# Kernel optimization log

Hardware: AMD Instinct MI355X
Metric: run time of the kernel (lower is better)

## Reference

```python
import jax, jax.numpy as jnp
import numpy as np

B, S, D, F_DIM, E, TOP_K = 4, 2048, 1024, 1024, 8, 2


def setup_inputs() -> dict:
    key = jax.random.key(0)
    ks = jax.random.split(key, 6)
    return {
        "x": jax.random.normal(ks[0], (B, S, D), jnp.float32),
        "router_w": jax.random.normal(ks[1], (E, D), jnp.float32) * 0.02,
        "router_b": jax.random.normal(ks[2], (E,), jnp.float32) * 0.02,
        "expert_w": jax.random.normal(ks[3], (E, F_DIM, D), jnp.float32) * 0.02,
        "expert_b": jax.random.normal(ks[4], (E, F_DIM), jnp.float32) * 0.02,
        "expert_pref": jax.random.normal(ks[5], (E, D), jnp.float32),
        "top_k": TOP_K,
    }


def reference(x, router_w, router_b, expert_w, expert_b, expert_pref, top_k):
    num_experts = expert_w.shape[0]
    # Router: softmax over experts, then top-k with renormalization
    logits = jnp.einsum("bsd,ed->bse", x, router_w) + router_b
    routing_weights = jax.nn.softmax(logits, axis=-1)            # [B,S,E]
    top_w, top_idx = jax.lax.top_k(routing_weights, top_k)       # [B,S,K]
    top_w = top_w / jnp.sum(top_w, axis=-1, keepdims=True)
    # Dense per-expert combine weight: sum of renormalized top-k weights routed to each expert
    onehot = jax.nn.one_hot(top_idx, num_experts, dtype=x.dtype)  # [B,S,K,E]
    comb = jnp.einsum("bske,bsk->bse", onehot, top_w)             # [B,S,E]
    # Per-expert linear for every token, weighted combine (dense grouped-GEMM form)
    expert_out = jnp.einsum("bsd,efd->bsef", x, expert_w) + expert_b  # [B,S,E,F]
    final_output = jnp.einsum("bsef,bse->bsf", expert_out, comb)      # [B,S,F]
    # Expert utilization: fraction of tokens whose top-k contains expert i
    mask = jnp.sum(onehot, axis=2) > 0                            # [B,S,E]
    expert_utilization = jnp.mean(mask.astype(x.dtype), axis=(0, 1))
    # Load balance loss: MSE of mean routing weight vs ideal uniform usage
    usage = jnp.mean(routing_weights, axis=(0, 1))
    load_balance_loss = jnp.mean((usage - 1.0 / num_experts) ** 2)
    # Diversity: mean pairwise L2 distance over concatenated expert params (fixed small E)
    flat = jnp.concatenate(
        [expert_w.reshape(num_experts, -1), expert_b, expert_pref], axis=1
    )  # [E, P]
    dists = [jnp.linalg.norm(flat[i] - flat[j])
             for i in range(num_experts) for j in range(i + 1, num_experts)]
    diversity_score = jnp.mean(jnp.stack(dists))
    return final_output, routing_weights, expert_utilization, load_balance_loss, diversity_score
```

## Files before the change

kernel.cpp:

```cpp
#include <hip/hip_runtime.h>
#include <stdint.h>

typedef unsigned short u16;
typedef __attribute__((ext_vector_type(4))) float f32x4;
typedef __attribute__((ext_vector_type(8))) short bf16x8;

#define NTOK 8192
#define DDIM 1024
#define FDIM 1024
#define NEXP 8
#define PCAP 8192
#define RBLK 512

__device__ __align__(256) u16 g_xb[NTOK * DDIM];
__device__ __align__(256) u16 g_wbf[NEXP * FDIM * DDIM];
__device__ __align__(256) u16 g_buf0[NTOK * FDIM];
__device__ __align__(256) u16 g_buf1[NTOK * FDIM];
__device__ __align__(256) int g_ptok[NEXP * PCAP];
__device__ __align__(256) float g_pw[NEXP * PCAP];
__device__ __align__(256) unsigned g_e01[NTOK];
__device__ __align__(256) float g_w0[NTOK];
__device__ __align__(256) float g_w1[NTOK];
__device__ __align__(256) float g_usage_part[NEXP * RBLK];
__device__ __align__(256) float g_gram_part[36 * RBLK];
__device__ __align__(256) unsigned g_tile[160];
__device__ int g_cnt[16];

__device__ __forceinline__ u16 f2bf(float f) {
  unsigned u = __builtin_bit_cast(unsigned, f);
  unsigned r = u + 0x7fffu + ((u >> 16) & 1u);
  return (u16)(r >> 16);
}

__device__ __forceinline__ float b2f(unsigned h) {
  return __builtin_bit_cast(float, h << 16);
}

__device__ __forceinline__ void gload_lds16(const void* g, void* l) {
  __builtin_amdgcn_global_load_lds(
      (const __attribute__((address_space(1))) void*)g,
      (__attribute__((address_space(3))) void*)l, 16, 0, 0);
}

__global__ __launch_bounds__(256) void k_pre(const float* __restrict__ x,
                                             const float* __restrict__ rwg,
                                             const float* __restrict__ rb,
                                             const float* __restrict__ ew,
                                             const float* __restrict__ ebias,
                                             const float* __restrict__ epref,
                                             float* __restrict__ rwout) {
  const int tid = threadIdx.x;
  if (blockIdx.x >= RBLK) {
    const int bid = blockIdx.x - RBLK;
    const int P0 = FDIM * DDIM;
    const int PT = P0 + FDIM + DDIM;
    float g[36];
#pragma unroll
    for (int i = 0; i < 36; ++i) g[i] = 0.f;
    for (int k = bid * 256 + tid; k < PT; k += RBLK * 256) {
      float v[8];
      if (k < P0) {
#pragma unroll
        for (int e = 0; e < 8; ++e) v[e] = ew[(size_t)e * P0 + k];
#pragma unroll
        for (int e = 0; e < 8; ++e) g_wbf[(size_t)e * P0 + k] = f2bf(v[e]);
      } else if (k < P0 + FDIM) {
        int kk = k - P0;
#pragma unroll
        for (int e = 0; e < 8; ++e) v[e] = ebias[e * FDIM + kk];
      } else {
        int kk = k - P0 - FDIM;
#pragma unroll
        for (int e = 0; e < 8; ++e) v[e] = epref[e * DDIM + kk];
      }
      int idx = 0;
#pragma unroll
      for (int i = 0; i < 8; ++i)
#pragma unroll
        for (int j = i; j < 8; ++j) {
          g[idx] += v[i] * v[j];
          ++idx;
        }
    }
#pragma unroll
    for (int i = 0; i < 36; ++i) {
      float a = g[i];
#pragma unroll
      for (int s = 32; s; s >>= 1) a += __shfl_xor(a, s);
      g[i] = a;
    }
    __shared__ float gs[4][36];
    const int w = tid >> 6, lane = tid & 63;
    if (lane == 0) {
#pragma unroll
      for (int i = 0; i < 36; ++i) gs[w][i] = g[i];
    }
    __syncthreads();
    if (tid < 36)
      g_gram_part[tid * RBLK + bid] =
          gs[0][tid] + gs[1][tid] + gs[2][tid] + gs[3][tid];
    return;
  }
  __shared__ __align__(16) float rw_lds[NEXP * DDIM];
  __shared__ float us[NEXP];
  const int w = tid >> 6, lane = tid & 63;
  {
    const float4* src = (const float4*)rwg;
    float4* dst = (float4*)rw_lds;
#pragma unroll
    for (int i = 0; i < 8; ++i) dst[tid + 256 * i] = src[tid + 256 * i];
  }
  if (tid < NEXP) us[tid] = 0.f;
  __syncthreads();

  float rbl[NEXP];
#pragma unroll
  for (int e = 0; e < NEXP; ++e) rbl[e] = rb[e];
  float uw[NEXP];
#pragma unroll
  for (int e = 0; e < NEXP; ++e) uw[e] = 0.f;

  for (int it = 0; it < 4; ++it) {
    const int t = blockIdx.x * 16 + w * 4 + it;
    const float4* xv = (const float4*)(x + (size_t)t * DDIM);
    float4 xv4[4];
#pragma unroll
    for (int j = 0; j < 4; ++j) xv4[j] = xv[lane + 64 * j];
    ushort4* xo = (ushort4*)(g_xb + (size_t)t * DDIM);
#pragma unroll
    for (int j = 0; j < 4; ++j) {
      float4 v = xv4[j];
      ushort4 o;
      o.x = f2bf(v.x); o.y = f2bf(v.y); o.z = f2bf(v.z); o.w = f2bf(v.w);
      xo[lane + 64 * j] = o;
    }
    float lg[NEXP];
#pragma unroll
    for (int e = 0; e < NEXP; ++e) {
      float a = 0.f;
#pragma unroll
      for (int j = 0; j < 4; ++j) {
        float4 r = *(const float4*)&rw_lds[e * DDIM + (lane + 64 * j) * 4];
        float4 v = xv4[j];
        a += v.x * r.x + v.y * r.y + v.z * r.z + v.w * r.w;
      }
      lg[e] = a;
    }
#pragma unroll
    for (int e = 0; e < NEXP; ++e) {
      float a = lg[e];
#pragma unroll
      for (int s = 32; s; s >>= 1) a += __shfl_xor(a, s);
      lg[e] = a + rbl[e];
    }
    float mx = lg[0];
#pragma unroll
    for (int e = 1; e < NEXP; ++e) mx = fmaxf(mx, lg[e]);
    float p[NEXP];
    float sm = 0.f;
#pragma unroll
    for (int e = 0; e < NEXP; ++e) {
      p[e] = expf(lg[e] - mx);
      sm += p[e];
    }
    float inv = 1.f / sm;
#pragma unroll
    for (int e = 0; e < NEXP; ++e) {
      p[e] *= inv;
      uw[e] += p[e];
    }
    int e0 = 0;
    float b0 = p[0];
#pragma unroll
    for (int e = 1; e < NEXP; ++e)
      if (p[e] > b0) { b0 = p[e]; e0 = e; }
    int e1 = -1;
    float b1 = -1.f;
#pragma unroll
    for (int e = 0; e < NEXP; ++e)
      if (e != e0 && p[e] > b1) { b1 = p[e]; e1 = e; }
    if (lane == 0) {
      float4* rw4 = (float4*)(rwout + (size_t)t * NEXP);
      rw4[0] = make_float4(p[0], p[1], p[2], p[3]);
      rw4[1] = make_float4(p[4], p[5], p[6], p[7]);
      float rn = 1.f / (b0 + b1);
      g_e01[t] = (unsigned)e0 | ((unsigned)e1 << 8);
      g_w0[t] = b0 * rn;
      g_w1[t] = b1 * rn;
    }
  }
  if (lane == 0) {
#pragma unroll
    for (int e = 0; e < NEXP; ++e) atomicAdd(&us[e], uw[e]);
  }
  __syncthreads();
  if (tid < NEXP) g_usage_part[tid * RBLK + blockIdx.x] = us[tid];
}

__global__ __launch_bounds__(256) void k_lists(float* __restrict__ out_util,
                                               float* __restrict__ out_lbl,
                                               float* __restrict__ out_div) {
  const int tid = threadIdx.x;
  const int wv = tid >> 6, lane = tid & 63;
  if (blockIdx.x == 8) {
    __shared__ int hw[4][8];
    __shared__ int hist[8];
    __shared__ int s_nt[8], s_placed[8];
    __shared__ float su[8];
    __shared__ float sg[36];
    int cnt[8];
#pragma unroll
    for (int e = 0; e < 8; ++e) cnt[e] = 0;
#pragma unroll 8
    for (int t = tid; t < NTOK; t += 256) {
      unsigned rec = g_e01[t];
      int ea = (int)(rec & 255u), ebx = (int)((rec >> 8) & 255u);
#pragma unroll
      for (int e = 0; e < 8; ++e) cnt[e] += (ea == e) + (ebx == e);
    }
#pragma unroll
    for (int e = 0; e < 8; ++e) {
      int a = cnt[e];
#pragma unroll
      for (int s = 32; s; s >>= 1) a += __shfl_xor(a, s);
      cnt[e] = a;
    }
    if (lane == 0) {
#pragma unroll
      for (int e = 0; e < 8; ++e) hw[wv][e] = cnt[e];
    }
    {
      int ue = tid >> 5, ul = tid & 31;
      float a = 0.f;
#pragma unroll
      for (int k = 0; k < 16; ++k) a += g_usage_part[ue * RBLK + ul + k * 32];
#pragma unroll
      for (int s = 16; s; s >>= 1) a += __shfl_xor(a, s);
      if (ul == 0) su[ue] = a;
    }
#pragma unroll
    for (int k = 0; k < 9; ++k) {
      int gi = wv + k * 4;
      float a = 0.f;
#pragma unroll
      for (int q = 0; q < 8; ++q) a += g_gram_part[gi * RBLK + lane + q * 64];
#pragma unroll
      for (int s = 32; s; s >>= 1) a += __shfl_xor(a, s);
      if (lane == 0) sg[gi] = a;
    }
    __syncthreads();
    if (tid < 8) {
      int h = hw[0][tid] + hw[1][tid] + hw[2][tid] + hw[3][tid];
      hist[tid] = h;
      s_nt[tid] = (h + 127) >> 7;
      s_placed[tid] = 0;
      out_util[tid] = (float)h * (1.f / 8192.f);
    }
    __syncthreads();
    if (tid == 0) {
      float dv = 0.f;
#pragma unroll
      for (int e = 0; e < 8; ++e) {
        float u = su[e] * (1.f / 8192.f) - 0.125f;
        dv += u * u;
      }
      out_lbl[0] = dv * 0.125f;
      for (int p = 0; p < 136; ++p) {
        int e = p & 7;
        if (s_placed[e] >= s_nt[e]) {
          e = -1;
          for (int f = 0; f < 8; ++f)
            if (s_placed[f] < s_nt[f]) { e = f; break; }
        }
        unsigned v = 0xFFFFFFFFu;
        if (e >= 0) {
          v = ((unsigned)e << 16) | (unsigned)s_placed[e];
          s_placed[e] = s_placed[e] + 1;
        }
        g_tile[p] = v;
      }
    }
    if (tid < 64) {
      float ds = 0.f;
      if (tid < 28) {
        int c = tid, i = 0;
        while (c >= 7 - i) { c -= 7 - i; ++i; }
        int j = i + 1 + c;
        auto tri = [](int a2, int b2) {
          return a2 * 8 - (a2 * (a2 - 1)) / 2 + (b2 - a2);
        };
        float d2 = sg[tri(i, i)] + sg[tri(j, j)] - 2.f * sg[tri(i, j)];
        ds = sqrtf(fmaxf(d2, 0.f));
      }
#pragma unroll
      for (int s = 16; s; s >>= 1) ds += __shfl_xor(ds, s);
      if (tid == 0) out_div[0] = ds * (1.f / 28.f);
    }
    return;
  }
  const int e = blockIdx.x;
  unsigned recs[32];
#pragma unroll
  for (int c = 0; c < 32; ++c) recs[c] = g_e01[c * 256 + tid];
  __shared__ int wcnt[2][4];
  int base = 0;
#pragma unroll
  for (int c = 0; c < 32; ++c) {
    const int t = c * 256 + tid;
    unsigned rec = recs[c];
    int m0 = (int)(rec & 255u) == e;
    int m1 = (int)((rec >> 8) & 255u) == e;
    unsigned long long bal = __ballot(m0 || m1);
    int rank = __popcll(bal & ((1ull << lane) - 1ull));
    if (lane == 0) wcnt[c & 1][wv] = __popcll(bal);
    __syncthreads();
    int pre = base;
#pragma unroll
    for (int i = 0; i < 4; ++i)
      if (i < wv) pre += wcnt[c & 1][i];
    int tot = wcnt[c & 1][0] + wcnt[c & 1][1] + wcnt[c & 1][2] + wcnt[c & 1][3];
    if (m0 || m1) {
      int idx = pre + rank;
      g_ptok[e * PCAP + idx] = (t << 1) | (m1 ? 1 : 0);
      g_pw[e * PCAP + idx] = m1 ? g_w1[t] : g_w0[t];
    }
    base += tot;
  }
  if (tid == 0) g_cnt[e] = base;
}

__global__ __launch_bounds__(512) void k_gemm(const float* __restrict__ eb) {
  const unsigned tl = g_tile[blockIdx.x];
  if (tl == 0xFFFFFFFFu) return;
  const int e = tl >> 16;
  const int count = g_cnt[e];
  const int m0 = (tl & 0xffffu) * 128;
  if (m0 >= count) return;
  const int n0 = blockIdx.y * 128;

  __shared__ __align__(16) u16 As[2][128 * 64];
  __shared__ __align__(16) u16 Bs[2][128 * 64];

  const int tid = threadIdx.x;
  const int lane = tid & 63;
  const int w = tid >> 6;
  const int wm = w >> 2, wn = w & 3;
  const int col16 = lane & 15, rg = lane >> 4;

  const int* ptok = g_ptok + e * PCAP;

  const u16* srcA[2];
  const u16* srcB[2];
  unsigned soff[2];
#pragma unroll
  for (int c = 0; c < 2; ++c) {
    int o = c * 8192 + tid * 16;
    int row = o >> 7;
    int sl = (o >> 4) & 7;
    int r = m0 + row;
    if (r > count - 1) r = count - 1;
    int tk = (ptok[r] >> 1) & (NTOK - 1);
    srcA[c] = g_xb + (size_t)tk * DDIM + ((sl ^ (row & 7)) << 3);
    srcB[c] = g_wbf + (size_t)e * (FDIM * DDIM) + (size_t)(n0 + row) * DDIM +
              ((sl ^ (row & 7)) << 3);
    soff[c] = (unsigned)o;
  }

#define STAGE(buf, k0)                                                        \
  {                                                                           \
    _Pragma("unroll") for (int c = 0; c < 2; ++c)                             \
        gload_lds16((const char*)(srcA[c] + (k0)), (char*)As[buf] + soff[c]); \
    _Pragma("unroll") for (int c = 0; c < 2; ++c)                             \
        gload_lds16((const char*)(srcB[c] + (k0)), (char*)Bs[buf] + soff[c]); \
  }

  f32x4 acc[4][2];
  const f32x4 zz = {0.f, 0.f, 0.f, 0.f};
#pragma unroll
  for (int i = 0; i < 4; ++i)
#pragma unroll
    for (int j = 0; j < 2; ++j) acc[i][j] = zz;

  STAGE(0, 0);
  STAGE(1, 64);

  const int sxor = col16 & 7;
  for (int kk = 0; kk < 16; ++kk) {
    const int cur = kk & 1;
    if (kk < 15) {
      asm volatile("s_waitcnt vmcnt(4)" ::: "memory");
    } else {
      asm volatile("s_waitcnt vmcnt(0)" ::: "memory");
    }
    __builtin_amdgcn_s_barrier();
    __builtin_amdgcn_sched_barrier(0);

#pragma unroll
    for (int ki = 0; ki < 2; ++ki) {
      bf16x8 af[4], bg[2];
#pragma unroll
      for (int mi = 0; mi < 4; ++mi) {
        int row = wm * 64 + mi * 16 + col16;
        af[mi] = *(const bf16x8*)(As[cur] + row * 64 +
                                  (((ki * 4 + rg) ^ sxor) << 3));
      }
#pragma unroll
      for (int ni = 0; ni < 2; ++ni) {
        int row = wn * 32 + ni * 16 + col16;
        bg[ni] = *(const bf16x8*)(Bs[cur] + row * 64 +
                                  (((ki * 4 + rg) ^ sxor) << 3));
      }
      __builtin_amdgcn_s_setprio(1);
#pragma unroll
      for (int mi = 0; mi < 4; ++mi)
#pragma unroll
        for (int ni = 0; ni < 2; ++ni)
          acc[mi][ni] = __builtin_amdgcn_mfma_f32_16x16x32_bf16(
              af[mi], bg[ni], acc[mi][ni], 0, 0, 0);
      __builtin_amdgcn_s_setprio(0);
    }

    asm volatile("" ::: "memory");
    __builtin_amdgcn_s_barrier();
    asm volatile("" ::: "memory");
    if (kk + 2 < 16) STAGE(cur, (kk + 2) * 64);
  }
#undef STAGE

#pragma unroll
  for (int mi = 0; mi < 4; ++mi) {
#pragma unroll
    for (int j = 0; j < 4; ++j) {
      int r = m0 + wm * 64 + mi * 16 + rg * 4 + j;
      if (r < count) {
        int enc = ptok[r];
        int tk = (enc >> 1) & (NTOK - 1);
        float wgt = g_pw[e * PCAP + r];
        u16* dst = (enc & 1 ? g_buf1 : g_buf0) + (size_t)tk * FDIM + n0 +
                   wn * 32 + col16;
        const float* bias = eb + e * FDIM + n0 + wn * 32 + col16;
#pragma unroll
        for (int ni = 0; ni < 2; ++ni)
          dst[ni * 16] = f2bf(wgt * (acc[mi][ni][j] + bias[ni * 16]));
      }
    }
  }
}

__global__ __launch_bounds__(256) void k_combine(float4* __restrict__ o, int n8) {
  const uint4* a = (const uint4*)g_buf0;
  const uint4* b = (const uint4*)g_buf1;
  int i = blockIdx.x * 256 + threadIdx.x;
  int stride = gridDim.x * 256;
  for (; i < n8; i += stride) {
    uint4 va = a[i], vb = b[i];
    float4 lo, hi;
    lo.x = b2f(va.x & 0xffffu) + b2f(vb.x & 0xffffu);
    lo.y = b2f(va.x >> 16) + b2f(vb.x >> 16);
    lo.z = b2f(va.y & 0xffffu) + b2f(vb.y & 0xffffu);
    lo.w = b2f(va.y >> 16) + b2f(vb.y >> 16);
    hi.x = b2f(va.z & 0xffffu) + b2f(vb.z & 0xffffu);
    hi.y = b2f(va.z >> 16) + b2f(vb.z >> 16);
    hi.z = b2f(va.w & 0xffffu) + b2f(vb.w & 0xffffu);
    hi.w = b2f(va.w >> 16) + b2f(vb.w >> 16);
    o[(size_t)i * 2] = lo;
    o[(size_t)i * 2 + 1] = hi;
  }
}

extern "C" void kernel_launch(void* const* d_in, const int* in_sizes, int n_in,
                              void* d_out, int out_size, void* d_ws,
                              size_t ws_size, hipStream_t stream) {
  const float* x = (const float*)d_in[0];
  const float* rwg = (const float*)d_in[1];
  const float* rb = (const float*)d_in[2];
  const float* ew = (const float*)d_in[3];
  const float* eb = (const float*)d_in[4];
  const float* ep = (const float*)d_in[5];

  float* out = (float*)d_out;
  float* out_final = out;
  float* out_rw = out + (size_t)NTOK * FDIM;
  float* out_util = out_rw + (size_t)NTOK * NEXP;
  float* out_lbl = out_util + NEXP;
  float* out_div = out_lbl + 1;

  k_pre<<<1024, 256, 0, stream>>>(x, rwg, rb, ew, eb, ep, out_rw);
  k_lists<<<9, 256, 0, stream>>>(out_util, out_lbl, out_div);
  k_gemm<<<dim3(136, 8), 512, 0, stream>>>(eb);
  k_combine<<<2048, 256, 0, stream>>>((float4*)out_final, (NTOK * FDIM) / 8);
}
```

Before: 127.4 us.

## Load expert weight fragments directly from global into registers, bypass LDS

Drops the shared-memory staging of the B (expert weight) tile and has each wave read its bf16 weight fragments straight from global memory into registers. The A tile keeps LDS double buffering, but the pipeline is simplified: one stage is prefetched per iteration after a plain __syncthreads, replacing the hand-tuned vmcnt waits and two-deep prefetch. This halves LDS usage and LDS traffic, which could raise occupancy. In exchange, each weight element is now loaded redundantly by the two wm waves, and global-load latency sits directly in front of the MFMAs with less prefetch depth.

```diff
diff --git a/kernel.cpp b/kernel.cpp
--- a/kernel.cpp
+++ b/kernel.cpp
@@ -339,7 +339,6 @@
   const int n0 = blockIdx.y * 128;
 
   __shared__ __align__(16) u16 As[2][128 * 64];
-  __shared__ __align__(16) u16 Bs[2][128 * 64];
 
   const int tid = threadIdx.x;
   const int lane = tid & 63;
@@ -350,7 +349,6 @@
   const int* ptok = g_ptok + e * PCAP;
 
   const u16* srcA[2];
-  const u16* srcB[2];
   unsigned soff[2];
 #pragma unroll
   for (int c = 0; c < 2; ++c) {
@@ -361,17 +359,17 @@
     if (r > count - 1) r = count - 1;
     int tk = (ptok[r] >> 1) & (NTOK - 1);
     srcA[c] = g_xb + (size_t)tk * DDIM + ((sl ^ (row & 7)) << 3);
-    srcB[c] = g_wbf + (size_t)e * (FDIM * DDIM) + (size_t)(n0 + row) * DDIM +
-              ((sl ^ (row & 7)) << 3);
     soff[c] = (unsigned)o;
   }
+
+  const u16* gB0 = g_wbf + (size_t)e * (FDIM * DDIM) +
+                   (size_t)(n0 + wn * 32 + col16) * DDIM;
+  const u16* gB1 = gB0 + (size_t)16 * DDIM;
 
 #define STAGE(buf, k0)                                                        \
   {                                                                           \
     _Pragma("unroll") for (int c = 0; c < 2; ++c)                             \
         gload_lds16((const char*)(srcA[c] + (k0)), (char*)As[buf] + soff[c]); \
-    _Pragma("unroll") for (int c = 0; c < 2; ++c)                             \
-        gload_lds16((const char*)(srcB[c] + (k0)), (char*)Bs[buf] + soff[c]); \
   }
 
   f32x4 acc[4][2];
@@ -382,34 +380,23 @@
     for (int j = 0; j < 2; ++j) acc[i][j] = zz;
 
   STAGE(0, 0);
-  STAGE(1, 64);
 
   const int sxor = col16 & 7;
   for (int kk = 0; kk < 16; ++kk) {
     const int cur = kk & 1;
-    if (kk < 15) {
-      asm volatile("s_waitcnt vmcnt(4)" ::: "memory");
-    } else {
-      asm volatile("s_waitcnt vmcnt(0)" ::: "memory");
-    }
-    __builtin_amdgcn_s_barrier();
-    __builtin_amdgcn_sched_barrier(0);
-
+    __syncthreads();
+    if (kk < 15) STAGE(cur ^ 1, (kk + 1) * 64);
 #pragma unroll
     for (int ki = 0; ki < 2; ++ki) {
       bf16x8 af[4], bg[2];
+      bg[0] = *(const bf16x8*)(gB0 + kk * 64 + ki * 32 + rg * 8);
+      bg[1] = *(const bf16x8*)(gB1 + kk * 64 + ki * 32 + rg * 8);
 #pragma unroll
       for (int mi = 0; mi < 4; ++mi) {
         int row = wm * 64 + mi * 16 + col16;
         af[mi] = *(const bf16x8*)(As[cur] + row * 64 +
                                   (((ki * 4 + rg) ^ sxor) << 3));
       }
-#pragma unroll
-      for (int ni = 0; ni < 2; ++ni) {
-        int row = wn * 32 + ni * 16 + col16;
-        bg[ni] = *(const bf16x8*)(Bs[cur] + row * 64 +
-                                  (((ki * 4 + rg) ^ sxor) << 3));
-      }
       __builtin_amdgcn_s_setprio(1);
 #pragma unroll
       for (int mi = 0; mi < 4; ++mi)
@@ -419,11 +406,6 @@
               af[mi], bg[ni], acc[mi][ni], 0, 0, 0);
       __builtin_amdgcn_s_setprio(0);
     }
-
-    asm volatile("" ::: "memory");
-    __builtin_amdgcn_s_barrier();
-    asm volatile("" ::: "memory");
-    if (kk + 2 < 16) STAGE(cur, (kk + 2) * 64);
   }
 #undef STAGE
 
```

Result: slower. 170.7 us (+34.0%).
